# Kernel tuning notes

Hardware: AMD Instinct MI355X
Metric: run time of the kernel (lower is better)

## Reference

```python
import jax, jax.numpy as jnp
import numpy as np

K = 9  # kernel_size (kNN neighbors, includes self since loop=True)


def _knn_edges(x_f, batch, k):
    # x_f: [N, C]. Full pairwise squared distances, masked across batch groups.
    N = x_f.shape[0]
    sq = jnp.sum(x_f * x_f, axis=1)
    d2 = sq[:, None] - 2.0 * (x_f @ x_f.T) + sq[None, :]          # [N, N]
    same = batch[:, None] == batch[None, :]
    d2 = jnp.where(same, d2, jnp.inf)
    neg_d, idx = jax.lax.top_k(-d2, k)                             # k nearest per query row
    valid = jnp.isfinite(neg_d)                                    # guard tiny groups (<k nodes)
    src = idx.reshape(-1)                                          # neighbor -> source
    tgt = jnp.repeat(jnp.arange(N), k)                             # query    -> target
    return src, tgt, valid.reshape(-1)


def _cheb_conv(x_f, src, tgt, valid, W0, W1, bias):
    # ChebConv, K=2, normalization='sym', lambda_max=2.0:
    #   out = x @ W0 + (L_hat x) @ W1 + b,  L_hat = -D^{-1/2} A D^{-1/2} (diag 0)
    N = x_f.shape[0]
    w = jnp.where(valid & (src != tgt), 1.0, 0.0)                  # remove_self_loops
    deg = jax.ops.segment_sum(w, src, num_segments=N)
    dis = jnp.where(deg > 0, jax.lax.rsqrt(jnp.maximum(deg, 1e-30)), 0.0)
    norm = -dis[src] * w * dis[tgt]                                # off-diag of scaled Laplacian
    Tx1 = jax.ops.segment_sum(norm[:, None] * x_f[src], tgt, num_segments=N)
    return x_f @ W0 + Tx1 @ W1 + bias


def setup_inputs() -> dict:
    key = jax.random.key(0)
    k1, k2, k3, k4 = jax.random.split(key, 4)
    B, C, H, W = 8, 192, 32, 32
    Cout = 192
    return {
        "x": jax.random.normal(k1, (B, C, H, W), dtype=jnp.float32),
        "W0": jax.random.normal(k2, (C, Cout), dtype=jnp.float32) * (1.0 / np.sqrt(C)),
        "W1": jax.random.normal(k3, (C, Cout), dtype=jnp.float32) * (1.0 / np.sqrt(C)),
        "bias": jax.random.normal(k4, (Cout,), dtype=jnp.float32) * 0.01,
    }


def reference(x, W0, W1, bias):
    B, C, H, W = x.shape
    N = B * H * W
    x_f = jnp.transpose(x, (0, 2, 3, 1)).reshape(N, C)             # flat_nodes: [B*H*W, C]
    # torch.linspace(0, B, steps=N, dtype=int64) -> truncated float linspace
    batch = jnp.linspace(0.0, float(B), N).astype(jnp.int32)
    src, tgt, valid = _knn_edges(x_f, batch, K)
    return _cheb_conv(x_f, src, tgt, valid, W0, W1, bias)
```

## Files before the change

kernel.cpp:

```cpp
#include <hip/hip_runtime.h>
#include <math.h>

#define NN 8192
#define CF 192
#define KNN 9
#define NSPL 8
#define PKS 12

typedef __bf16 v8bf __attribute__((ext_vector_type(8)));
typedef float f32x16 __attribute__((ext_vector_type(16)));
typedef float f32x4 __attribute__((ext_vector_type(4)));

__device__ __forceinline__ int group_start(int g) {
    int s = (8191 * g + 7) >> 3;
    return s > 8192 ? 8192 : s;
}

__device__ __forceinline__ float disf(int d) {
    return d > 0 ? 1.0f / sqrtf((float)d) : 0.0f;
}

__device__ __forceinline__ unsigned short f2bf(float f) {
    unsigned u = __float_as_uint(f);
    unsigned r = (u + 0x7FFFu + ((u >> 16) & 1u)) >> 16;
    return (unsigned short)r;
}
__device__ __forceinline__ float bf2f(unsigned short h) {
    return __uint_as_float(((unsigned)h) << 16);
}

__global__ __launch_bounds__(256) void transpose_kernel(
    const float* __restrict__ x, unsigned short* __restrict__ xh,
    unsigned short* __restrict__ xl, float* __restrict__ sq,
    int* __restrict__ deg)
{
    __shared__ float tile[32][33];
    int b = blockIdx.x, ht = blockIdx.y;
    int hw0 = ht * 32;
    int tid = threadIdx.x;
    if (tid < 32) deg[b * 1024 + hw0 + tid] = 0;

    float sacc[4];
#pragma unroll
    for (int p = 0; p < 4; ++p) sacc[p] = 0.0f;

    for (int ct = 0; ct < 6; ++ct) {
        int c0 = ct * 32;
        __syncthreads();
#pragma unroll
        for (int p = 0; p < 4; ++p) {
            int c  = p * 8 + (tid >> 5);
            int hw = tid & 31;
            tile[c][hw] = x[(size_t)b * 196608 + (size_t)(c0 + c) * 1024 + hw0 + hw];
        }
        __syncthreads();
#pragma unroll
        for (int p = 0; p < 4; ++p) {
            int hw = p * 8 + (tid >> 5);
            int cc = tid & 31;
            float v = tile[cc][hw];
            size_t o = (size_t)(b * 1024 + hw0 + hw) * CF + c0 + cc;
            unsigned short h = f2bf(v);
            xh[o] = h;
            xl[o] = f2bf(v - bf2f(h));
            sacc[p] = fmaf(v, v, sacc[p]);
        }
    }
#pragma unroll
    for (int p = 0; p < 4; ++p) {
        float s = sacc[p];
#pragma unroll
        for (int off = 16; off > 0; off >>= 1) s += __shfl_xor(s, off, 32);
        if ((tid & 31) == 0)
            sq[(size_t)(b * 1024 + hw0 + p * 8 + (tid >> 5))] = s;
    }
}

__global__ __launch_bounds__(256, 2) void knn_kernel(
    const unsigned short* __restrict__ xh, const unsigned short* __restrict__ xl,
    const float* __restrict__ sq,
    float* __restrict__ pk_d, int* __restrict__ pk_i)
{
    int bid = blockIdx.x;
    int g = bid >> 7;
    int rem = bid & 127;
    int qb = rem >> 3;
    int split = rem & 7;
    int gs = group_start(g);
    int gsize = group_start(g + 1) - gs;
    int q0 = qb * 64;
    int nq = gsize - q0; if (nq > 64) nq = 64;
    if (nq <= 0) return;
    int c0 = split * 128;
    int ncc = gsize - c0; if (ncc > 128) ncc = 128;

    int tid = threadIdx.x;

    if (ncc <= 0) {
        if (tid < nq) {
            int q = gs + q0 + tid;
            size_t base = ((size_t)q * NSPL + split) * PKS;
#pragma unroll
            for (int j = 0; j < KNN; ++j) { pk_d[base + j] = __builtin_inff(); pk_i[base + j] = -1; }
        }
        return;
    }

    __shared__ __align__(16) char smem[55296];
    unsigned short* sm = (unsigned short*)smem;
    __shared__ float sqc_s[128];
    __shared__ float sqq_s[64];

    int lane = tid & 63, w = tid >> 6;
    int arow = (w & 1) * 32 + (lane & 31);
    int k8 = (lane >> 5) * 8;
    int brow0 = (w >> 1) * 64 + (lane & 31);

    if (tid < 64) {
        int qo = q0 + tid; if (qo > gsize - 1) qo = gsize - 1;
        sqq_s[tid] = sq[gs + qo];
    }
    if (tid < 128) {
        sqc_s[tid] = (tid < ncc) ? sq[gs + c0 + tid] : __builtin_inff();
    }

    int rr = tid >> 2, q4 = tid & 3;
    int aq = q0 + rr; if (aq > gsize - 1) aq = gsize - 1;
    int cqA = c0 + rr;      if (cqA > gsize - 1) cqA = gsize - 1;
    int cqB = c0 + 64 + rr; if (cqB > gsize - 1) cqB = gsize - 1;
    int g0 = (gs + aq)  * CF + q4 * 16;
    int g1 = g0 + NN * CF;
    int g2 = (gs + cqA) * CF + q4 * 16;
    int g3 = (gs + cqB) * CF + q4 * 16;
    int g4 = g2 + NN * CF;
    int g5 = g3 + NN * CF;
    int s0 = rr * 72 + q4 * 16;
    int s1 = s0 + 4608;
    int s2 = 9216 + rr * 72 + q4 * 16;
    int s3 = s2 + 4608;
    int s4 = s2 + 9216;
    int s5 = s3 + 9216;

    f32x16 acc[2];
#pragma unroll
    for (int t = 0; t < 2; ++t)
#pragma unroll
        for (int r = 0; r < 16; ++r) acc[t][r] = 0.0f;

    uint4 d0a, d0b, d1a, d1b, d2a, d2b, d3a, d3b, d4a, d4b, d5a, d5b;
    d0a = *(const uint4*)(xh + g0); d0b = *(const uint4*)(xh + g0 + 8);
    d1a = *(const uint4*)(xh + g1); d1b = *(const uint4*)(xh + g1 + 8);
    d2a = *(const uint4*)(xh + g2); d2b = *(const uint4*)(xh + g2 + 8);
    d3a = *(const uint4*)(xh + g3); d3b = *(const uint4*)(xh + g3 + 8);
    d4a = *(const uint4*)(xh + g4); d4b = *(const uint4*)(xh + g4 + 8);
    d5a = *(const uint4*)(xh + g5); d5b = *(const uint4*)(xh + g5 + 8);

    for (int kb = 0; kb < 3; ++kb) {
        *(uint4*)(sm + s0) = d0a; *(uint4*)(sm + s0 + 8) = d0b;
        *(uint4*)(sm + s1) = d1a; *(uint4*)(sm + s1 + 8) = d1b;
        *(uint4*)(sm + s2) = d2a; *(uint4*)(sm + s2 + 8) = d2b;
        *(uint4*)(sm + s3) = d3a; *(uint4*)(sm + s3 + 8) = d3b;
        *(uint4*)(sm + s4) = d4a; *(uint4*)(sm + s4 + 8) = d4b;
        *(uint4*)(sm + s5) = d5a; *(uint4*)(sm + s5 + 8) = d5b;
        __syncthreads();
        if (kb < 2) {
            int o = (kb + 1) * 64;
            d0a = *(const uint4*)(xh + g0 + o); d0b = *(const uint4*)(xh + g0 + o + 8);
            d1a = *(const uint4*)(xh + g1 + o); d1b = *(const uint4*)(xh + g1 + o + 8);
            d2a = *(const uint4*)(xh + g2 + o); d2b = *(const uint4*)(xh + g2 + o + 8);
            d3a = *(const uint4*)(xh + g3 + o); d3b = *(const uint4*)(xh + g3 + o + 8);
            d4a = *(const uint4*)(xh + g4 + o); d4b = *(const uint4*)(xh + g4 + o + 8);
            d5a = *(const uint4*)(xh + g5 + o); d5b = *(const uint4*)(xh + g5 + o + 8);
        }
#pragma unroll
        for (int h = 0; h < 4; ++h) {
            int ao = arow * 72 + h * 16 + k8;
            v8bf a_hi = *(const v8bf*)(sm + ao);
            v8bf a_lo = *(const v8bf*)(sm + 4608 + ao);
#pragma unroll
            for (int t = 0; t < 2; ++t) {
                int bo = 9216 + (brow0 + t * 32) * 72 + h * 16 + k8;
                v8bf b_hi = *(const v8bf*)(sm + bo);
                v8bf b_lo = *(const v8bf*)(sm + 9216 + bo);
                acc[t] = __builtin_amdgcn_mfma_f32_32x32x16_bf16(a_hi, b_hi, acc[t], 0, 0, 0);
                acc[t] = __builtin_amdgcn_mfma_f32_32x32x16_bf16(a_lo, b_hi, acc[t], 0, 0, 0);
                acc[t] = __builtin_amdgcn_mfma_f32_32x32x16_bf16(a_hi, b_lo, acc[t], 0, 0, 0);
            }
        }
        __syncthreads();
    }

    float (*Ds)[133] = (float(*)[133])smem;
#pragma unroll
    for (int t = 0; t < 2; ++t)
#pragma unroll
        for (int r = 0; r < 16; ++r) {
            int row = (w & 1) * 32 + (r & 3) + 8 * (r >> 2) + 4 * (lane >> 5);
            int col = (w >> 1) * 64 + t * 32 + (lane & 31);
            Ds[row][col] = acc[t][r];
        }
    __syncthreads();

    int qq = tid >> 2, ch = tid & 3;
    float sqqv = sqq_s[qq];
    float pd[KNN]; int pi[KNN];
#pragma unroll
    for (int j = 0; j < KNN; ++j) { pd[j] = __builtin_inff(); pi[j] = -1; }
#pragma unroll
    for (int qt = 0; qt < 4; ++qt) {
        float dv[8], cv[8];
#pragma unroll
        for (int j8 = 0; j8 < 8; ++j8) {
            int c = ch * 32 + qt * 8 + j8;
            dv[j8] = Ds[qq][c];
            cv[j8] = sqc_s[c];
        }
#pragma unroll
        for (int j8 = 0; j8 < 8; ++j8) {
            float d = (sqqv - 2.0f * dv[j8]) + cv[j8];
            if (d < pd[KNN - 1]) {
                pd[KNN - 1] = d; pi[KNN - 1] = gs + c0 + ch * 32 + qt * 8 + j8;
#pragma unroll
                for (int j = KNN - 1; j > 0; --j) {
                    if (pd[j] < pd[j - 1]) {
                        float tf = pd[j]; pd[j] = pd[j - 1]; pd[j - 1] = tf;
                        int tn = pi[j]; pi[j] = pi[j - 1]; pi[j - 1] = tn;
                    }
                }
            }
        }
    }

#define MERGE_ROUND(MASK, SELBIT)                                              \
    {                                                                          \
        float od[KNN]; int oi[KNN];                                            \
        _Pragma("unroll")                                                      \
        for (int j = 0; j < KNN; ++j) {                                        \
            od[j] = __shfl_xor(pd[j], MASK);                                   \
            oi[j] = __shfl_xor(pi[j], MASK);                                   \
        }                                                                      \
        bool swp = (ch & SELBIT) != 0;                                         \
        float ad[KNN]; int ai[KNN]; float bd[KNN]; int bi[KNN];                \
        _Pragma("unroll")                                                      \
        for (int j = 0; j < KNN; ++j) {                                        \
            ad[j] = swp ? od[j] : pd[j];  ai[j] = swp ? oi[j] : pi[j];         \
            bd[j] = swp ? pd[j] : od[j];  bi[j] = swp ? pi[j] : oi[j];         \
        }                                                                      \
        _Pragma("unroll")                                                      \
        for (int j0 = 0; j0 < KNN; ++j0) {                                     \
            float d = bd[j0];                                                  \
            if (!(d < ad[KNN - 1])) break;      \
            ad[KNN - 1] = d; ai[KNN - 1] = bi[j0];                             \
            _Pragma("unroll")                                                  \
            for (int j = KNN - 1; j > 0; --j) {                                \
                if (ad[j] < ad[j - 1]) {                                       \
                    float tf = ad[j]; ad[j] = ad[j - 1]; ad[j - 1] = tf;       \
                    int tn = ai[j]; ai[j] = ai[j - 1]; ai[j - 1] = tn;         \
                }                                                              \
            }                                                                  \
        }                                                                      \
        _Pragma("unroll")                                                      \
        for (int j = 0; j < KNN; ++j) { pd[j] = ad[j]; pi[j] = ai[j]; }        \
    }
    MERGE_ROUND(1, 1)
    MERGE_ROUND(2, 2)
#undef MERGE_ROUND

    if (ch == 0 && qq < nq) {
        int q = gs + q0 + qq;
        size_t base = ((size_t)q * NSPL + split) * PKS;
#pragma unroll
        for (int j = 0; j < KNN; ++j) { pk_d[base + j] = pd[j]; pk_i[base + j] = pi[j]; }
    }
}

__global__ __launch_bounds__(64) void merge_kernel(
    const float* __restrict__ pk_d, const int* __restrict__ pk_i,
    int* __restrict__ edges, int* __restrict__ deg,
    const float* __restrict__ W0, const float* __restrict__ W1,
    unsigned short* __restrict__ wt)
{
    __shared__ float wtile[32][33];
    int tid = threadIdx.x;
    if (blockIdx.x >= 128) {
        int wid = blockIdx.x - 128;
        int mat = wid / 36, rem2 = wid % 36;
        int k0 = (rem2 / 6) * 32, n0 = (rem2 % 6) * 32;
        const float* W = mat ? W1 : W0;
#pragma unroll
        for (int p = 0; p < 4; ++p) {
            int idx = p * 64 + tid;
            int k = idx >> 3, n4 = (idx & 7) * 4;
            *(float4*)&wtile[k][n4] =
                *(const float4*)(W + (size_t)(k0 + k) * CF + n0 + n4);
        }
        __syncthreads();
#pragma unroll
        for (int p = 0; p < 4; ++p) {
            int idx = p * 64 + tid;
            int n = idx >> 3, k4 = (idx & 7) * 4;
            ushort4 h;
            h.x = f2bf(wtile[k4 + 0][n]); h.y = f2bf(wtile[k4 + 1][n]);
            h.z = f2bf(wtile[k4 + 2][n]); h.w = f2bf(wtile[k4 + 3][n]);
            *(ushort4*)(wt + (size_t)mat * 36864 + (size_t)(n0 + n) * CF + k0 + k4) = h;
        }
        return;
    }
    int q = blockIdx.x * 64 + tid;
    float td[KNN]; int ti[KNN];
#pragma unroll
    for (int j = 0; j < KNN; ++j) { td[j] = __builtin_inff(); ti[j] = -1; }
#pragma unroll
    for (int sb = 0; sb < 2; ++sb) {
        float sd[4][KNN]; int si[4][KNN];
#pragma unroll
        for (int s2 = 0; s2 < 4; ++s2) {
            int s = sb * 4 + s2;
            const float* pd = pk_d + ((size_t)q * NSPL + s) * PKS;
            const int*   pp = pk_i + ((size_t)q * NSPL + s) * PKS;
            float4 d0 = *(const float4*)pd;
            float4 d1 = *(const float4*)(pd + 4);
            sd[s2][0] = d0.x; sd[s2][1] = d0.y; sd[s2][2] = d0.z; sd[s2][3] = d0.w;
            sd[s2][4] = d1.x; sd[s2][5] = d1.y; sd[s2][6] = d1.z; sd[s2][7] = d1.w;
            sd[s2][8] = pd[8];
            int4 i0 = *(const int4*)pp;
            int4 i1 = *(const int4*)(pp + 4);
            si[s2][0] = i0.x; si[s2][1] = i0.y; si[s2][2] = i0.z; si[s2][3] = i0.w;
            si[s2][4] = i1.x; si[s2][5] = i1.y; si[s2][6] = i1.z; si[s2][7] = i1.w;
            si[s2][8] = pp[8];
        }
#pragma unroll
        for (int s2 = 0; s2 < 4; ++s2) {
#pragma unroll
            for (int j0 = 0; j0 < KNN; ++j0) {
                float d = sd[s2][j0];
                if (!(d < td[KNN - 1])) break;
                td[KNN - 1] = d; ti[KNN - 1] = si[s2][j0];
#pragma unroll
                for (int j = KNN - 1; j > 0; --j) {
                    if (td[j] < td[j - 1]) {
                        float tf = td[j]; td[j] = td[j - 1]; td[j - 1] = tf;
                        int tn = ti[j]; ti[j] = ti[j - 1]; ti[j - 1] = tn;
                    }
                }
            }
        }
    }
#pragma unroll
    for (int j = 0; j < KNN; ++j) {
        int id = ti[j];
        edges[q * KNN + j] = id;
        if (id >= 0 && id != q) atomicAdd(&deg[id], 1);
    }
}

__global__ __launch_bounds__(256, 2) void out_kernel(
    const unsigned short* __restrict__ xh, const unsigned short* __restrict__ wt,
    const int* __restrict__ edges, const int* __restrict__ deg,
    const float* __restrict__ bias, float* __restrict__ out)
{
    __shared__ __align__(16) unsigned short A0s[16][200];
    __shared__ __align__(16) unsigned short A1s[16][200];
    __shared__ unsigned short Wts[2][CF][32];
    __shared__ float coef_s[16][KNN];
    __shared__ int   nb_s[16][KNN];
    unsigned short* wts = &Wts[0][0][0];

    int r0 = blockIdx.x * 16;
    int tid = threadIdx.x;

    int wb0, wb1, wb2, wb3, wb4, wb5;
    int ws0, ws1, ws2, ws3, ws4, ws5;
#define WROLE(P, GB, SB)                                                       \
    {                                                                          \
        int f = (P) * 256 + tid;                                               \
        int mat = f / 768, n = (f % 768) / 4, k16 = (f % 4) * 8;               \
        GB = mat * 36864 + n * CF + k16;                                       \
        SB = mat * 6144 + n * 32 + k16;                                        \
    }
    WROLE(0, wb0, ws0) WROLE(1, wb1, ws1) WROLE(2, wb2, ws2)
    WROLE(3, wb3, ws3) WROLE(4, wb4, ws4) WROLE(5, wb5, ws5)
#undef WROLE
    uint4 wr0 = *(const uint4*)(wt + wb0);
    uint4 wr1 = *(const uint4*)(wt + wb1);
    uint4 wr2 = *(const uint4*)(wt + wb2);
    uint4 wr3 = *(const uint4*)(wt + wb3);
    uint4 wr4 = *(const uint4*)(wt + wb4);
    uint4 wr5 = *(const uint4*)(wt + wb5);

    for (int t = tid; t < 384; t += 256) {
        int i = t / 24, c8 = (t % 24) * 8;
        *(uint4*)&A0s[i][c8] = *(const uint4*)(xh + (size_t)(r0 + i) * CF + c8);
    }
    if (tid < 16 * KNN) {
        int i = tid / KNN, j = tid % KNN;
        int q = r0 + i;
        int id = edges[q * KNN + j];
        float cf = 0.0f; int s = q;
        if (id >= 0 && id != q) { cf = -disf(deg[id]) * disf(deg[q]); s = id; }
        coef_s[i][j] = cf; nb_s[i][j] = s;
    }
    __syncthreads();
    for (int e = tid; e < 16 * CF / 8; e += 256) {
        int i = e / 24, c8 = (e % 24) * 8;
        float a[8];
#pragma unroll
        for (int j = 0; j < 8; ++j) a[j] = 0.0f;
#pragma unroll
        for (int t = 0; t < KNN; ++t) {
            float cf = coef_s[i][t];
            uint4 v = *(const uint4*)(xh + (size_t)nb_s[i][t] * CF + c8);
            const unsigned short* pv = (const unsigned short*)&v;
#pragma unroll
            for (int j = 0; j < 8; ++j) a[j] = fmaf(cf, bf2f(pv[j]), a[j]);
        }
        uint4 hv;
        hv.x = (unsigned)f2bf(a[0]) | ((unsigned)f2bf(a[1]) << 16);
        hv.y = (unsigned)f2bf(a[2]) | ((unsigned)f2bf(a[3]) << 16);
        hv.z = (unsigned)f2bf(a[4]) | ((unsigned)f2bf(a[5]) << 16);
        hv.w = (unsigned)f2bf(a[6]) | ((unsigned)f2bf(a[7]) << 16);
        *(uint4*)&A1s[i][c8] = hv;
    }

    int lane = tid & 63, w = tid >> 6;
    int m = lane & 15;
    int kq = (lane >> 4) * 8;
    f32x4 acc[3];
#pragma unroll
    for (int t = 0; t < 3; ++t)
#pragma unroll
        for (int r = 0; r < 4; ++r) acc[t][r] = 0.0f;

    for (int kt = 0; kt < 6; ++kt) {
        __syncthreads();
        *(uint4*)(wts + ws0) = wr0;
        *(uint4*)(wts + ws1) = wr1;
        *(uint4*)(wts + ws2) = wr2;
        *(uint4*)(wts + ws3) = wr3;
        *(uint4*)(wts + ws4) = wr4;
        *(uint4*)(wts + ws5) = wr5;
        __syncthreads();
        if (kt < 5) {
            int o = (kt + 1) * 32;
            wr0 = *(const uint4*)(wt + wb0 + o);
            wr1 = *(const uint4*)(wt + wb1 + o);
            wr2 = *(const uint4*)(wt + wb2 + o);
            wr3 = *(const uint4*)(wt + wb3 + o);
            wr4 = *(const uint4*)(wt + wb4 + o);
            wr5 = *(const uint4*)(wt + wb5 + o);
        }
        v8bf a0 = *(const v8bf*)&A0s[m][kt * 32 + kq];
        v8bf a1 = *(const v8bf*)&A1s[m][kt * 32 + kq];
#pragma unroll
        for (int t3 = 0; t3 < 3; ++t3) {
            int n0 = w * 48 + t3 * 16;
            v8bf w0 = *(const v8bf*)(wts + (n0 + m) * 32 + kq);
            v8bf w1 = *(const v8bf*)(wts + 6144 + (n0 + m) * 32 + kq);
            acc[t3] = __builtin_amdgcn_mfma_f32_16x16x32_bf16(a0, w0, acc[t3], 0, 0, 0);
            acc[t3] = __builtin_amdgcn_mfma_f32_16x16x32_bf16(a1, w1, acc[t3], 0, 0, 0);
        }
    }

    int col = lane & 15, rb = (lane >> 4) * 4;
#pragma unroll
    for (int t3 = 0; t3 < 3; ++t3) {
        int n0 = w * 48 + t3 * 16;
        float bv = bias[n0 + col];
#pragma unroll
        for (int r = 0; r < 4; ++r)
            out[(size_t)(r0 + rb + r) * CF + n0 + col] = acc[t3][r] + bv;
    }
}

extern "C" void kernel_launch(void* const* d_in, const int* in_sizes, int n_in,
                              void* d_out, int out_size, void* d_ws, size_t ws_size,
                              hipStream_t stream)
{
    const float* x    = (const float*)d_in[0];
    const float* W0   = (const float*)d_in[1];
    const float* W1   = (const float*)d_in[2];
    const float* bias = (const float*)d_in[3];
    float* out = (float*)d_out;

    char* ws = (char*)d_ws;
    unsigned short* xh = (unsigned short*)ws; ws += (size_t)NN * CF * 2;
    unsigned short* xl = (unsigned short*)ws; ws += (size_t)NN * CF * 2;
    float* sq    = (float*)ws;  ws += (size_t)NN * 4;
    int*   deg   = (int*)ws;    ws += (size_t)NN * 4;
    int*   edges = (int*)ws;    ws += (size_t)NN * KNN * 4;

    unsigned short* wt = xl;

    float* pk_d = out;
    int*   pk_i = (int*)(out + (size_t)NN * NSPL * PKS);

    hipLaunchKernelGGL(transpose_kernel, dim3(8, 32), dim3(256), 0, stream,
                       x, xh, xl, sq, deg);
    hipLaunchKernelGGL(knn_kernel, dim3(1152), dim3(256), 0, stream,
                       xh, xl, sq, pk_d, pk_i);
    hipLaunchKernelGGL(merge_kernel, dim3(200), dim3(64), 0, stream,
                       pk_d, pk_i, edges, deg, W0, W1, wt);
    hipLaunchKernelGGL(out_kernel, dim3(512), dim3(256), 0, stream,
                       xh, wt, edges, deg, bias, out);
}
```

Measured before the change: 133.4 us.

## Enlarge kNN query tile to 128 rows with thinner K-slices and two-pass top-k

```diff
diff --git a/kernel.cpp b/kernel.cpp
--- a/kernel.cpp
+++ b/kernel.cpp
@@ -82,14 +82,14 @@
     float* __restrict__ pk_d, int* __restrict__ pk_i)
 {
     int bid = blockIdx.x;
-    int g = bid >> 7;
-    int rem = bid & 127;
+    int g = bid >> 6;
+    int rem = bid & 63;
     int qb = rem >> 3;
     int split = rem & 7;
     int gs = group_start(g);
     int gsize = group_start(g + 1) - gs;
-    int q0 = qb * 64;
-    int nq = gsize - q0; if (nq > 64) nq = 64;
+    int q0 = qb * 128;
+    int nq = gsize - q0; if (nq > 128) nq = 128;
     if (nq <= 0) return;
     int c0 = split * 128;
     int ncc = gsize - c0; if (ncc > 128) ncc = 128;
@@ -106,82 +106,68 @@
         return;
     }
 
-    __shared__ __align__(16) char smem[55296];
+    __shared__ __align__(16) char smem[40960];
     unsigned short* sm = (unsigned short*)smem;
     __shared__ float sqc_s[128];
-    __shared__ float sqq_s[64];
+    __shared__ float sqq_s[128];
 
     int lane = tid & 63, w = tid >> 6;
-    int arow = (w & 1) * 32 + (lane & 31);
+    int arow = w * 32 + (lane & 31);
     int k8 = (lane >> 5) * 8;
-    int brow0 = (w >> 1) * 64 + (lane & 31);
-
-    if (tid < 64) {
+
+    if (tid < 128) {
         int qo = q0 + tid; if (qo > gsize - 1) qo = gsize - 1;
         sqq_s[tid] = sq[gs + qo];
-    }
-    if (tid < 128) {
         sqc_s[tid] = (tid < ncc) ? sq[gs + c0 + tid] : __builtin_inff();
     }
 
-    int rr = tid >> 2, q4 = tid & 3;
+    int rr = tid >> 1, half = tid & 1;
     int aq = q0 + rr; if (aq > gsize - 1) aq = gsize - 1;
-    int cqA = c0 + rr;      if (cqA > gsize - 1) cqA = gsize - 1;
-    int cqB = c0 + 64 + rr; if (cqB > gsize - 1) cqB = gsize - 1;
-    int g0 = (gs + aq)  * CF + q4 * 16;
-    int g1 = g0 + NN * CF;
-    int g2 = (gs + cqA) * CF + q4 * 16;
-    int g3 = (gs + cqB) * CF + q4 * 16;
-    int g4 = g2 + NN * CF;
-    int g5 = g3 + NN * CF;
-    int s0 = rr * 72 + q4 * 16;
-    int s1 = s0 + 4608;
-    int s2 = 9216 + rr * 72 + q4 * 16;
-    int s3 = s2 + 4608;
-    int s4 = s2 + 9216;
-    int s5 = s3 + 9216;
-
-    f32x16 acc[2];
-#pragma unroll
-    for (int t = 0; t < 2; ++t)
+    int cq = c0 + rr; if (cq > gsize - 1) cq = gsize - 1;
+    int gA = (gs + aq) * CF + half * 16;
+    int gL = gA + NN * CF;
+    int gB = (gs + cq) * CF + half * 16;
+    int gC = gB + NN * CF;
+    int sA = rr * 40 + half * 16;
+    int sL = sA + 5120;
+    int sB = 10240 + rr * 40 + half * 16;
+    int sC = sB + 5120;
+
+    f32x16 acc[4];
+#pragma unroll
+    for (int t = 0; t < 4; ++t)
 #pragma unroll
         for (int r = 0; r < 16; ++r) acc[t][r] = 0.0f;
 
-    uint4 d0a, d0b, d1a, d1b, d2a, d2b, d3a, d3b, d4a, d4b, d5a, d5b;
-    d0a = *(const uint4*)(xh + g0); d0b = *(const uint4*)(xh + g0 + 8);
-    d1a = *(const uint4*)(xh + g1); d1b = *(const uint4*)(xh + g1 + 8);
-    d2a = *(const uint4*)(xh + g2); d2b = *(const uint4*)(xh + g2 + 8);
-    d3a = *(const uint4*)(xh + g3); d3b = *(const uint4*)(xh + g3 + 8);
-    d4a = *(const uint4*)(xh + g4); d4b = *(const uint4*)(xh + g4 + 8);
-    d5a = *(const uint4*)(xh + g5); d5b = *(const uint4*)(xh + g5 + 8);
-
-    for (int kb = 0; kb < 3; ++kb) {
-        *(uint4*)(sm + s0) = d0a; *(uint4*)(sm + s0 + 8) = d0b;
-        *(uint4*)(sm + s1) = d1a; *(uint4*)(sm + s1 + 8) = d1b;
-        *(uint4*)(sm + s2) = d2a; *(uint4*)(sm + s2 + 8) = d2b;
-        *(uint4*)(sm + s3) = d3a; *(uint4*)(sm + s3 + 8) = d3b;
-        *(uint4*)(sm + s4) = d4a; *(uint4*)(sm + s4 + 8) = d4b;
-        *(uint4*)(sm + s5) = d5a; *(uint4*)(sm + s5 + 8) = d5b;
-        __syncthreads();
-        if (kb < 2) {
-            int o = (kb + 1) * 64;
-            d0a = *(const uint4*)(xh + g0 + o); d0b = *(const uint4*)(xh + g0 + o + 8);
-            d1a = *(const uint4*)(xh + g1 + o); d1b = *(const uint4*)(xh + g1 + o + 8);
-            d2a = *(const uint4*)(xh + g2 + o); d2b = *(const uint4*)(xh + g2 + o + 8);
-            d3a = *(const uint4*)(xh + g3 + o); d3b = *(const uint4*)(xh + g3 + o + 8);
-            d4a = *(const uint4*)(xh + g4 + o); d4b = *(const uint4*)(xh + g4 + o + 8);
-            d5a = *(const uint4*)(xh + g5 + o); d5b = *(const uint4*)(xh + g5 + o + 8);
-        }
-#pragma unroll
-        for (int h = 0; h < 4; ++h) {
-            int ao = arow * 72 + h * 16 + k8;
+    uint4 rA0, rA1, rL0, rL1, rB0, rB1, rC0, rC1;
+    rA0 = *(const uint4*)(xh + gA); rA1 = *(const uint4*)(xh + gA + 8);
+    rL0 = *(const uint4*)(xh + gL); rL1 = *(const uint4*)(xh + gL + 8);
+    rB0 = *(const uint4*)(xh + gB); rB1 = *(const uint4*)(xh + gB + 8);
+    rC0 = *(const uint4*)(xh + gC); rC1 = *(const uint4*)(xh + gC + 8);
+
+    for (int kb = 0; kb < 6; ++kb) {
+        *(uint4*)(sm + sA) = rA0; *(uint4*)(sm + sA + 8) = rA1;
+        *(uint4*)(sm + sL) = rL0; *(uint4*)(sm + sL + 8) = rL1;
+        *(uint4*)(sm + sB) = rB0; *(uint4*)(sm + sB + 8) = rB1;
+        *(uint4*)(sm + sC) = rC0; *(uint4*)(sm + sC + 8) = rC1;
+        __syncthreads();
+        if (kb < 5) {
+            int o = (kb + 1) * 32;
+            rA0 = *(const uint4*)(xh + gA + o); rA1 = *(const uint4*)(xh + gA + o + 8);
+            rL0 = *(const uint4*)(xh + gL + o); rL1 = *(const uint4*)(xh + gL + o + 8);
+            rB0 = *(const uint4*)(xh + gB + o); rB1 = *(const uint4*)(xh + gB + o + 8);
+            rC0 = *(const uint4*)(xh + gC + o); rC1 = *(const uint4*)(xh + gC + o + 8);
+        }
+#pragma unroll
+        for (int h = 0; h < 2; ++h) {
+            int ao = arow * 40 + h * 16 + k8;
             v8bf a_hi = *(const v8bf*)(sm + ao);
-            v8bf a_lo = *(const v8bf*)(sm + 4608 + ao);
-#pragma unroll
-            for (int t = 0; t < 2; ++t) {
-                int bo = 9216 + (brow0 + t * 32) * 72 + h * 16 + k8;
+            v8bf a_lo = *(const v8bf*)(sm + 5120 + ao);
+#pragma unroll
+            for (int t = 0; t < 4; ++t) {
+                int bo = 10240 + (t * 32 + (lane & 31)) * 40 + h * 16 + k8;
                 v8bf b_hi = *(const v8bf*)(sm + bo);
-                v8bf b_lo = *(const v8bf*)(sm + 9216 + bo);
+                v8bf b_lo = *(const v8bf*)(sm + 5120 + bo);
                 acc[t] = __builtin_amdgcn_mfma_f32_32x32x16_bf16(a_hi, b_hi, acc[t], 0, 0, 0);
                 acc[t] = __builtin_amdgcn_mfma_f32_32x32x16_bf16(a_lo, b_hi, acc[t], 0, 0, 0);
                 acc[t] = __builtin_amdgcn_mfma_f32_32x32x16_bf16(a_hi, b_lo, acc[t], 0, 0, 0);
@@ -191,86 +177,91 @@
     }
 
     float (*Ds)[133] = (float(*)[133])smem;
-#pragma unroll
-    for (int t = 0; t < 2; ++t)
-#pragma unroll
-        for (int r = 0; r < 16; ++r) {
-            int row = (w & 1) * 32 + (r & 3) + 8 * (r >> 2) + 4 * (lane >> 5);
-            int col = (w >> 1) * 64 + t * 32 + (lane & 31);
-            Ds[row][col] = acc[t][r];
-        }
-    __syncthreads();
-
     int qq = tid >> 2, ch = tid & 3;
-    float sqqv = sqq_s[qq];
-    float pd[KNN]; int pi[KNN];
-#pragma unroll
-    for (int j = 0; j < KNN; ++j) { pd[j] = __builtin_inff(); pi[j] = -1; }
-#pragma unroll
-    for (int qt = 0; qt < 4; ++qt) {
-        float dv[8], cv[8];
-#pragma unroll
-        for (int j8 = 0; j8 < 8; ++j8) {
-            int c = ch * 32 + qt * 8 + j8;
-            dv[j8] = Ds[qq][c];
-            cv[j8] = sqc_s[c];
-        }
-#pragma unroll
-        for (int j8 = 0; j8 < 8; ++j8) {
-            float d = (sqqv - 2.0f * dv[j8]) + cv[j8];
-            if (d < pd[KNN - 1]) {
-                pd[KNN - 1] = d; pi[KNN - 1] = gs + c0 + ch * 32 + qt * 8 + j8;
-#pragma unroll
-                for (int j = KNN - 1; j > 0; --j) {
-                    if (pd[j] < pd[j - 1]) {
-                        float tf = pd[j]; pd[j] = pd[j - 1]; pd[j - 1] = tf;
-                        int tn = pi[j]; pi[j] = pi[j - 1]; pi[j - 1] = tn;
+#pragma unroll
+    for (int h = 0; h < 2; ++h) {
+        __syncthreads();
+        if ((w >> 1) == h) {
+#pragma unroll
+            for (int t = 0; t < 4; ++t)
+#pragma unroll
+                for (int r = 0; r < 16; ++r) {
+                    int row = (w & 1) * 32 + (r & 3) + 8 * (r >> 2) + 4 * (lane >> 5);
+                    Ds[row][t * 32 + (lane & 31)] = acc[t][r];
+                }
+        }
+        __syncthreads();
+
+        float sqqv = sqq_s[h * 64 + qq];
+        float pd[KNN]; int pi[KNN];
+#pragma unroll
+        for (int j = 0; j < KNN; ++j) { pd[j] = __builtin_inff(); pi[j] = -1; }
+#pragma unroll
+        for (int qt = 0; qt < 4; ++qt) {
+            float dv[8], cv[8];
+#pragma unroll
+            for (int j8 = 0; j8 < 8; ++j8) {
+                int c = ch * 32 + qt * 8 + j8;
+                dv[j8] = Ds[qq][c];
+                cv[j8] = sqc_s[c];
+            }
+#pragma unroll
+            for (int j8 = 0; j8 < 8; ++j8) {
+                float d = (sqqv - 2.0f * dv[j8]) + cv[j8];
+                if (d < pd[KNN - 1]) {
+                    pd[KNN - 1] = d; pi[KNN - 1] = gs + c0 + ch * 32 + qt * 8 + j8;
+#pragma unroll
+                    for (int j = KNN - 1; j > 0; --j) {
+                        if (pd[j] < pd[j - 1]) {
+                            float tf = pd[j]; pd[j] = pd[j - 1]; pd[j - 1] = tf;
+                            int tn = pi[j]; pi[j] = pi[j - 1]; pi[j - 1] = tn;
+                        }
                     }
                 }
             }
         }
-    }
 
 #define MERGE_ROUND(MASK, SELBIT)                                              \
-    {                                                                          \
-        float od[KNN]; int oi[KNN];                                            \
-        _Pragma("unroll")                                                      \
-        for (int j = 0; j < KNN; ++j) {                                        \
-            od[j] = __shfl_xor(pd[j], MASK);                                   \
-            oi[j] = __shfl_xor(pi[j], MASK);                                   \
-        }                                                                      \
-        bool swp = (ch & SELBIT) != 0;                                         \
-        float ad[KNN]; int ai[KNN]; float bd[KNN]; int bi[KNN];                \
-        _Pragma("unroll")                                                      \
-        for (int j = 0; j < KNN; ++j) {                                        \
-            ad[j] = swp ? od[j] : pd[j];  ai[j] = swp ? oi[j] : pi[j];         \
-            bd[j] = swp ? pd[j] : od[j];  bi[j] = swp ? pi[j] : oi[j];         \
-        }                                                                      \
-        _Pragma("unroll")                                                      \
-        for (int j0 = 0; j0 < KNN; ++j0) {                                     \
-            float d = bd[j0];                                                  \
-            if (!(d < ad[KNN - 1])) break;      \
-            ad[KNN - 1] = d; ai[KNN - 1] = bi[j0];                             \
+        {                                                                      \
+            float od[KNN]; int oi[KNN];                                        \
             _Pragma("unroll")                                                  \
-            for (int j = KNN - 1; j > 0; --j) {                                \
-                if (ad[j] < ad[j - 1]) {                                       \
-                    float tf = ad[j]; ad[j] = ad[j - 1]; ad[j - 1] = tf;       \
-                    int tn = ai[j]; ai[j] = ai[j - 1]; ai[j - 1] = tn;         \
+            for (int j = 0; j < KNN; ++j) {                                    \
+                od[j] = __shfl_xor(pd[j], MASK);                               \
+                oi[j] = __shfl_xor(pi[j], MASK);                               \
+            }                                                                  \
+            bool swp = (ch & SELBIT) != 0;                                     \
+            float ad[KNN]; int ai[KNN]; float bd[KNN]; int bi[KNN];            \
+            _Pragma("unroll")                                                  \
+            for (int j = 0; j < KNN; ++j) {                                    \
+                ad[j] = swp ? od[j] : pd[j];  ai[j] = swp ? oi[j] : pi[j];     \
+                bd[j] = swp ? pd[j] : od[j];  bi[j] = swp ? pi[j] : oi[j];     \
+            }                                                                  \
+            _Pragma("unroll")                                                  \
+            for (int j0 = 0; j0 < KNN; ++j0) {                                 \
+                float d = bd[j0];                                              \
+                if (!(d < ad[KNN - 1])) break;                                 \
+                ad[KNN - 1] = d; ai[KNN - 1] = bi[j0];                         \
+                _Pragma("unroll")                                              \
+                for (int j = KNN - 1; j > 0; --j) {                            \
+                    if (ad[j] < ad[j - 1]) {                                   \
+                        float tf = ad[j]; ad[j] = ad[j - 1]; ad[j - 1] = tf;   \
+                        int tn = ai[j]; ai[j] = ai[j - 1]; ai[j - 1] = tn;     \
+                    }                                                          \
                 }                                                              \
             }                                                                  \
-        }                                                                      \
-        _Pragma("unroll")                                                      \
-        for (int j = 0; j < KNN; ++j) { pd[j] = ad[j]; pi[j] = ai[j]; }        \
-    }
-    MERGE_ROUND(1, 1)
-    MERGE_ROUND(2, 2)
+            _Pragma("unroll")                                                  \
+            for (int j = 0; j < KNN; ++j) { pd[j] = ad[j]; pi[j] = ai[j]; }    \
+        }
+        MERGE_ROUND(1, 1)
+        MERGE_ROUND(2, 2)
 #undef MERGE_ROUND
 
-    if (ch == 0 && qq < nq) {
-        int q = gs + q0 + qq;
-        size_t base = ((size_t)q * NSPL + split) * PKS;
-#pragma unroll
-        for (int j = 0; j < KNN; ++j) { pk_d[base + j] = pd[j]; pk_i[base + j] = pi[j]; }
+        if (ch == 0 && h * 64 + qq < nq) {
+            int q = gs + q0 + h * 64 + qq;
+            size_t base = ((size_t)q * NSPL + split) * PKS;
+#pragma unroll
+            for (int j = 0; j < KNN; ++j) { pk_d[base + j] = pd[j]; pk_i[base + j] = pi[j]; }
+        }
     }
 }
 
@@ -496,7 +487,7 @@
 
     hipLaunchKernelGGL(transpose_kernel, dim3(8, 32), dim3(256), 0, stream,
                        x, xh, xl, sq, deg);
-    hipLaunchKernelGGL(knn_kernel, dim3(1152), dim3(256), 0, stream,
+    hipLaunchKernelGGL(knn_kernel, dim3(576), dim3(256), 0, stream,
                        xh, xl, sq, pk_d, pk_i);
     hipLaunchKernelGGL(merge_kernel, dim3(200), dim3(64), 0, stream,
                        pk_d, pk_i, edges, deg, W0, W1, wt);
```

Result: faster. 130.4 us (-2.2%).
